# Performance work log

Measured on AMD Instinct MI355X. Metric: run time of the kernel, lower is better.

The kernel has to match this reference:

```python
import jax, jax.numpy as jnp
import numpy as np

NEG_BIG = -1.0e9


def setup_inputs() -> dict:
    key = jax.random.key(0)
    ks = jax.random.split(key, 8)
    B, N, D = 4, 384, 256
    s = 1.0 / np.sqrt(D)
    return {
        "q": jax.random.normal(ks[0], (B, N, D), dtype=jnp.float32),
        "k": jax.random.normal(ks[1], (B, N, D), dtype=jnp.float32),
        "v": jax.random.normal(ks[2], (B, N, D), dtype=jnp.float32),
        "mask": jax.random.randint(ks[3], (B, 1, N, N), 0, 2, dtype=jnp.int32),
        "Wq": jax.random.normal(ks[4], (D, D), dtype=jnp.float32) * s,
        "bq": jnp.zeros((D,), dtype=jnp.float32),
        "Wk": jax.random.normal(ks[5], (D, D), dtype=jnp.float32) * s,
        "bk": jnp.zeros((D,), dtype=jnp.float32),
        "Wv": jax.random.normal(ks[6], (D, D), dtype=jnp.float32) * s,
        "bv": jnp.zeros((D,), dtype=jnp.float32),
    }


def reference(q, k, v, mask, Wq, bq, Wk, bk, Wv, bv):
    # Dense projections
    query = q @ Wq + bq   # [B, N, D]
    key_p = k @ Wk + bk   # [B, M, D]
    value = v @ Wv + bv   # [B, M, D]
    # Per-channel outer-product scores: [B, D, N, M]
    score = jnp.einsum('bnd,bmd->bdnm', query, key_p)
    score = score + mask.astype(score.dtype) * NEG_BIG  # mask broadcasts [B,1,N,M]
    weights = jnp.tanh(score)
    # Per-channel weighted sum back to [B, N, D]
    out = jnp.einsum('bdnm,bmd->bnd', weights, value)
    return out
```

## Files before the change

### kernel.cpp

```cpp
#include <hip/hip_runtime.h>

#define DD 256
#define NN 384
#define BB 4
#define BN (BB * NN)
#define MSPLIT 4
#define MCHUNK (NN / MSPLIT)

constexpr float TWO_LOG2E = 2.8853900817779268f;
constexpr float MASK_X    = -1.0e9f * 2.8853900817779268f;

__global__ __launch_bounds__(256) void proj_kernel(
    const float* __restrict__ q,  const float* __restrict__ k,  const float* __restrict__ v,
    const float* __restrict__ Wq, const float* __restrict__ Wk, const float* __restrict__ Wv,
    const float* __restrict__ bq, const float* __restrict__ bk, const float* __restrict__ bv,
    float* __restrict__ Qout, float* __restrict__ KVout)
{
    const int tid  = threadIdx.x;
    const int row0 = blockIdx.x * 8;
    const int which = blockIdx.y;

    const float* X; const float* W; const float* bias; float scale; float* out; int ostride;
    if (which == 0)      { X = q; W = Wq; bias = bq; scale = 1.0f;      out = Qout;      ostride = 1; }
    else if (which == 1) { X = k; W = Wk; bias = bk; scale = TWO_LOG2E; out = KVout;     ostride = 2; }
    else                 { X = v; W = Wv; bias = bv; scale = 1.0f;      out = KVout + 1; ostride = 2; }

    __shared__ float xs[8][DD];
    #pragma unroll
    for (int r = 0; r < 8; ++r)
        xs[r][tid] = X[(row0 + r) * DD + tid];
    __syncthreads();

    float acc[8] = {0.f,0.f,0.f,0.f,0.f,0.f,0.f,0.f};
    #pragma unroll 2
    for (int k0 = 0; k0 < DD; k0 += 8) {
        float w[8];
        #pragma unroll
        for (int j = 0; j < 8; ++j)
            w[j] = W[(k0 + j) * DD + tid];
        #pragma unroll
        for (int r = 0; r < 8; ++r) {
            const float4 xa = *reinterpret_cast<const float4*>(&xs[r][k0]);
            const float4 xb = *reinterpret_cast<const float4*>(&xs[r][k0 + 4]);
            acc[r] = fmaf(xa.x, w[0], acc[r]);
            acc[r] = fmaf(xa.y, w[1], acc[r]);
            acc[r] = fmaf(xa.z, w[2], acc[r]);
            acc[r] = fmaf(xa.w, w[3], acc[r]);
            acc[r] = fmaf(xb.x, w[4], acc[r]);
            acc[r] = fmaf(xb.y, w[5], acc[r]);
            acc[r] = fmaf(xb.z, w[6], acc[r]);
            acc[r] = fmaf(xb.w, w[7], acc[r]);
        }
    }
    const float bb = bias[tid];
    #pragma unroll
    for (int r = 0; r < 8; ++r)
        out[((row0 + r) * DD + tid) * ostride] = (acc[r] + bb) * scale;
}

__global__ __launch_bounds__(256, 6) void mhsa_kernel(
    const float* __restrict__ Q, const float* __restrict__ KV,
    const int* __restrict__ mask, float* __restrict__ out)
{
    const int tid = threadIdx.x;
    const int b   = blockIdx.y;
    const int n0  = blockIdx.x * 4;
    const int m0  = blockIdx.z * MCHUNK;

    __shared__ float mf[MCHUNK * 4];
    for (int idx = tid; idx < MCHUNK * 4; idx += 256) {
        const int m = idx % MCHUNK;
        const int j = idx / MCHUNK;
        mf[m * 4 + j] = mask[(b * NN + n0 + j) * NN + (m0 + m)] ? MASK_X : 0.0f;
    }
    __syncthreads();

    float qv[4];
    #pragma unroll
    for (int j = 0; j < 4; ++j)
        qv[j] = Q[(b * NN + n0 + j) * DD + tid];

    const float2* kvp = reinterpret_cast<const float2*>(KV)
                      + (size_t)b * NN * DD + (size_t)m0 * DD + tid;

    float acc[4] = {0.f, 0.f, 0.f, 0.f};
    #pragma unroll 2
    for (int mg = 0; mg < MCHUNK; mg += 8) {
        float2 kv[8];
        #pragma unroll
        for (int u = 0; u < 8; ++u)
            kv[u] = kvp[(size_t)(mg + u) * DD];
        #pragma unroll
        for (int u = 0; u < 8; ++u) {
            const float4 m4 = *reinterpret_cast<const float4*>(&mf[(mg + u) * 4]);
            const float mfj[4] = {m4.x, m4.y, m4.z, m4.w};
            #pragma unroll
            for (int j = 0; j < 4; ++j) {
                const float x = fmaf(qv[j], kv[u].x, mfj[j]);
                const float E = __builtin_amdgcn_exp2f(x);
                const float r = __builtin_amdgcn_rcpf(E + 1.0f);
                acc[j] += fmaf(-2.0f * kv[u].y, r, kv[u].y);
            }
        }
    }
    #pragma unroll
    for (int j = 0; j < 4; ++j)
        atomicAdd(&out[(b * NN + n0 + j) * DD + tid], acc[j]);
}

extern "C" void kernel_launch(void* const* d_in, const int* in_sizes, int n_in,
                              void* d_out, int out_size, void* d_ws, size_t ws_size,
                              hipStream_t stream) {
    const float* q    = (const float*)d_in[0];
    const float* k    = (const float*)d_in[1];
    const float* v    = (const float*)d_in[2];
    const int*   mask = (const int*)  d_in[3];
    const float* Wq   = (const float*)d_in[4];
    const float* bq   = (const float*)d_in[5];
    const float* Wk   = (const float*)d_in[6];
    const float* bk   = (const float*)d_in[7];
    const float* Wv   = (const float*)d_in[8];
    const float* bv   = (const float*)d_in[9];
    float* out = (float*)d_out;

    float* Qws  = (float*)d_ws;
    float* KVws = Qws + (size_t)BN * DD;

    hipMemsetAsync(d_out, 0, (size_t)out_size * sizeof(float), stream);

    dim3 g1(BN / 8, 3);
    proj_kernel<<<g1, 256, 0, stream>>>(q, k, v, Wq, Wk, Wv, bq, bk, bv, Qws, KVws);

    dim3 g2(NN / 4, BB, MSPLIT);
    mhsa_kernel<<<g2, 256, 0, stream>>>(Qws, KVws, mask, out);
}
```

Baseline: 130.9 us.

## Branch on mask to skip tanh, replace atomics with partial buffers and reduce

Masked entries now take a branch that subtracts the value directly instead of evaluating exp/rcp, and the mask is read per element from global memory instead of being staged in shared memory. The atomicAdd accumulation and memset are replaced by per-split partial output buffers followed by a separate reduction kernel. The projection kernel drops its shared-memory staging of X and reads it directly from global memory. The mask is random, so the branch diverges within wavefronts and both paths may execute, and the extra kernel launch adds traffic for the partial buffers.

```diff
diff --git a/kernel.cpp b/kernel.cpp
--- a/kernel.cpp
+++ b/kernel.cpp
@@ -6,9 +6,9 @@
 #define BN (BB * NN)
 #define MSPLIT 4
 #define MCHUNK (NN / MSPLIT)
+#define PSTRIDE (BN * DD)
 
 constexpr float TWO_LOG2E = 2.8853900817779268f;
-constexpr float MASK_X    = -1.0e9f * 2.8853900817779268f;
 
 __global__ __launch_bounds__(256) void proj_kernel(
     const float* __restrict__ q,  const float* __restrict__ k,  const float* __restrict__ v,
@@ -25,31 +25,21 @@
     else if (which == 1) { X = k; W = Wk; bias = bk; scale = TWO_LOG2E; out = KVout;     ostride = 2; }
     else                 { X = v; W = Wv; bias = bv; scale = 1.0f;      out = KVout + 1; ostride = 2; }
 
-    __shared__ float xs[8][DD];
-    #pragma unroll
-    for (int r = 0; r < 8; ++r)
-        xs[r][tid] = X[(row0 + r) * DD + tid];
-    __syncthreads();
+    const float* Xr = X + (size_t)row0 * DD;
 
     float acc[8] = {0.f,0.f,0.f,0.f,0.f,0.f,0.f,0.f};
     #pragma unroll 2
-    for (int k0 = 0; k0 < DD; k0 += 8) {
-        float w[8];
-        #pragma unroll
-        for (int j = 0; j < 8; ++j)
-            w[j] = W[(k0 + j) * DD + tid];
+    for (int k0 = 0; k0 < DD; k0 += 4) {
+        float w0 = W[(k0 + 0) * DD + tid];
+        float w1 = W[(k0 + 1) * DD + tid];
+        float w2 = W[(k0 + 2) * DD + tid];
+        float w3 = W[(k0 + 3) * DD + tid];
         #pragma unroll
         for (int r = 0; r < 8; ++r) {
-            const float4 xa = *reinterpret_cast<const float4*>(&xs[r][k0]);
-            const float4 xb = *reinterpret_cast<const float4*>(&xs[r][k0 + 4]);
-            acc[r] = fmaf(xa.x, w[0], acc[r]);
-            acc[r] = fmaf(xa.y, w[1], acc[r]);
-            acc[r] = fmaf(xa.z, w[2], acc[r]);
-            acc[r] = fmaf(xa.w, w[3], acc[r]);
-            acc[r] = fmaf(xb.x, w[4], acc[r]);
-            acc[r] = fmaf(xb.y, w[5], acc[r]);
-            acc[r] = fmaf(xb.z, w[6], acc[r]);
-            acc[r] = fmaf(xb.w, w[7], acc[r]);
+            acc[r] = fmaf(Xr[r * DD + k0 + 0], w0, acc[r]);
+            acc[r] = fmaf(Xr[r * DD + k0 + 1], w1, acc[r]);
+            acc[r] = fmaf(Xr[r * DD + k0 + 2], w2, acc[r]);
+            acc[r] = fmaf(Xr[r * DD + k0 + 3], w3, acc[r]);
         }
     }
     const float bb = bias[tid];
@@ -60,52 +50,59 @@
 
 __global__ __launch_bounds__(256, 6) void mhsa_kernel(
     const float* __restrict__ Q, const float* __restrict__ KV,
-    const int* __restrict__ mask, float* __restrict__ out)
+    const int* __restrict__ mask, float* __restrict__ outp)
 {
     const int tid = threadIdx.x;
     const int b   = blockIdx.y;
     const int n0  = blockIdx.x * 4;
     const int m0  = blockIdx.z * MCHUNK;
 
-    __shared__ float mf[MCHUNK * 4];
-    for (int idx = tid; idx < MCHUNK * 4; idx += 256) {
-        const int m = idx % MCHUNK;
-        const int j = idx / MCHUNK;
-        mf[m * 4 + j] = mask[(b * NN + n0 + j) * NN + (m0 + m)] ? MASK_X : 0.0f;
-    }
-    __syncthreads();
-
     float qv[4];
     #pragma unroll
     for (int j = 0; j < 4; ++j)
         qv[j] = Q[(b * NN + n0 + j) * DD + tid];
 
+    const int* mrow[4];
+    #pragma unroll
+    for (int j = 0; j < 4; ++j)
+        mrow[j] = mask + (size_t)(b * NN + n0 + j) * NN + m0;
+
     const float2* kvp = reinterpret_cast<const float2*>(KV)
                       + (size_t)b * NN * DD + (size_t)m0 * DD + tid;
 
     float acc[4] = {0.f, 0.f, 0.f, 0.f};
-    #pragma unroll 2
-    for (int mg = 0; mg < MCHUNK; mg += 8) {
-        float2 kv[8];
+    for (int mg = 0; mg < MCHUNK; mg += 4) {
+        float2 kv[4];
         #pragma unroll
-        for (int u = 0; u < 8; ++u)
+        for (int u = 0; u < 4; ++u)
             kv[u] = kvp[(size_t)(mg + u) * DD];
         #pragma unroll
-        for (int u = 0; u < 8; ++u) {
-            const float4 m4 = *reinterpret_cast<const float4*>(&mf[(mg + u) * 4]);
-            const float mfj[4] = {m4.x, m4.y, m4.z, m4.w};
+        for (int u = 0; u < 4; ++u) {
             #pragma unroll
             for (int j = 0; j < 4; ++j) {
-                const float x = fmaf(qv[j], kv[u].x, mfj[j]);
-                const float E = __builtin_amdgcn_exp2f(x);
-                const float r = __builtin_amdgcn_rcpf(E + 1.0f);
-                acc[j] += fmaf(-2.0f * kv[u].y, r, kv[u].y);
+                if (mrow[j][mg + u]) {
+                    acc[j] -= kv[u].y;
+                } else {
+                    const float x = qv[j] * kv[u].x;
+                    const float E = __builtin_amdgcn_exp2f(x);
+                    const float r = __builtin_amdgcn_rcpf(E + 1.0f);
+                    acc[j] += fmaf(-2.0f * kv[u].y, r, kv[u].y);
+                }
             }
         }
     }
+    float* po = outp + (size_t)blockIdx.z * PSTRIDE;
     #pragma unroll
     for (int j = 0; j < 4; ++j)
-        atomicAdd(&out[(b * NN + n0 + j) * DD + tid], acc[j]);
+        po[(b * NN + n0 + j) * DD + tid] = acc[j];
+}
+
+__global__ __launch_bounds__(256) void reduce4_kernel(
+    const float* __restrict__ part, float* __restrict__ out)
+{
+    const int i = blockIdx.x * 256 + threadIdx.x;
+    out[i] = (part[i] + part[i + PSTRIDE])
+           + (part[i + 2 * PSTRIDE] + part[i + 3 * PSTRIDE]);
 }
 
 extern "C" void kernel_launch(void* const* d_in, const int* in_sizes, int n_in,
@@ -123,14 +120,15 @@
     const float* bv   = (const float*)d_in[9];
     float* out = (float*)d_out;
 
-    float* Qws  = (float*)d_ws;
-    float* KVws = Qws + (size_t)BN * DD;
-
-    hipMemsetAsync(d_out, 0, (size_t)out_size * sizeof(float), stream);
+    float* Qws   = (float*)d_ws;
+    float* KVws  = Qws  + (size_t)BN * DD;
+    float* Pws   = KVws + (size_t)2 * BN * DD;
 
     dim3 g1(BN / 8, 3);
     proj_kernel<<<g1, 256, 0, stream>>>(q, k, v, Wq, Wk, Wv, bq, bk, bv, Qws, KVws);
 
     dim3 g2(NN / 4, BB, MSPLIT);
-    mhsa_kernel<<<g2, 256, 0, stream>>>(Qws, KVws, mask, out);
+    mhsa_kernel<<<g2, 256, 0, stream>>>(Qws, KVws, mask, Pws);
+
+    reduce4_kernel<<<dim3(BN * DD / 256), 256, 0, stream>>>(Pws, out);
 }
```

New measurement: 145.9 us. +11.5%, slower.
